# Kernel optimization log

Hardware: AMD Instinct MI355X
Metric: run time of the kernel (lower is better)

The kernel has to match this reference:

```python
import jax, jax.numpy as jnp
import numpy as np

B, N, D, Kp = 32, 4096, 128, 256  # batch*heads, seq_len, head_dim, linformer proj dim


def setup_inputs() -> dict:
    key = jax.random.key(0)
    ks = jax.random.split(key, 7)
    return {
        "Q": jax.random.normal(ks[0], (B, N, D), dtype=jnp.float32),
        "K": jax.random.normal(ks[1], (B, N, D), dtype=jnp.float32),
        "V": jax.random.normal(ks[2], (B, N, D), dtype=jnp.float32),
        "E_W": jax.random.normal(ks[3], (Kp, N), dtype=jnp.float32) * (1.0 / np.sqrt(N)),
        "E_b": jax.random.normal(ks[4], (Kp,), dtype=jnp.float32) * 0.02,
        "F_W": jax.random.normal(ks[5], (Kp, N), dtype=jnp.float32) * (1.0 / np.sqrt(N)),
        "F_b": jax.random.normal(ks[6], (Kp,), dtype=jnp.float32) * 0.02,
    }


def reference(Q, K, V, E_W, E_b, F_W, F_b):
    d = Q.shape[-1]
    scale = 1.0 / jnp.sqrt(jnp.asarray(d, Q.dtype))
    # E projection on K^T: [B,d,n] @ W^T -> [B,d,k]
    K_proj = jnp.einsum('bnd,kn->bdk', K, E_W) + E_b  # bias broadcasts over k axis
    # scaled scores [B,n,k], softmax over projected dim k
    scores = jnp.einsum('bnd,bdk->bnk', Q, K_proj) * scale
    P_bar = jax.nn.softmax(scores, axis=-1)
    # F projection on V^T then transpose back: [B,k,d]
    V_proj = jnp.einsum('bnd,kn->bkd', V, F_W) + F_b[:, None]
    # [B,n,k] @ [B,k,d] -> [B,n,d]
    return jnp.einsum('bnk,bkd->bnd', P_bar, V_proj)
```

## Files before the change

### kernel.cpp

```cpp
#include <hip/hip_runtime.h>
#include <cstdint>
#include <cstddef>

#define N_SEQ 4096
#define D_HEAD 128
#define KP_DIM 256

typedef __attribute__((ext_vector_type(4))) float f32x4;
typedef __attribute__((ext_vector_type(8))) short bf16x8;
typedef __attribute__((ext_vector_type(4))) short s16x4;
typedef __attribute__((ext_vector_type(2))) unsigned int u32x2;

static __device__ __forceinline__ short f2bf(float f) {
  uint32_t u = __builtin_bit_cast(uint32_t, f);
  u += 0x7FFFu + ((u >> 16) & 1u);
  return (short)(u >> 16);
}

static __device__ __forceinline__ unsigned int cvtpk(float a, float b) {
  unsigned int r;
  asm("v_cvt_pk_bf16_f32 %0, %1, %2" : "=v"(r) : "v"(a), "v"(b));
  return r;
}

static __device__ __forceinline__ int swz8(int r) { return (r ^ (r >> 2)) & 7; }

__global__ __launch_bounds__(256) void conv_w_kernel(
    const float* __restrict__ EW, const float* __restrict__ FW,
    short* __restrict__ wbf) {
  const int idx = blockIdx.x * 256 + threadIdx.x;
  const int half = 262144;
  f32x4 v = (idx < half) ? *(const f32x4*)(EW + (size_t)idx * 4)
                         : *(const f32x4*)(FW + (size_t)(idx - half) * 4);
  u32x2 h = {cvtpk(v[0], v[1]), cvtpk(v[2], v[3])};
  *(u32x2*)(wbf + (size_t)idx * 4) = h;
}

__global__ __launch_bounds__(1024, 4) void proj_partial_kernel(
    const float* __restrict__ Kin, const float* __restrict__ Vin,
    const short* __restrict__ wbf, float* __restrict__ pws) {
  const int bid = blockIdx.x;
  const int wk = (bid & 7) * 32 + (bid >> 3);
  const int b = wk & 31;
  const int s = (wk >> 5) & 3;
  const int p = wk >> 7;

  const float* __restrict__ X = (p == 0 ? Kin : Vin) + (size_t)b * (N_SEQ * D_HEAD);
  const short* __restrict__ wp = wbf + (size_t)p * (KP_DIM * N_SEQ);
  float* __restrict__ outp = pws + ((((size_t)b * 2 + p) * 4) + s) * (KP_DIM * D_HEAD);

  __shared__ __align__(16) short lw[2][KP_DIM * 64];
  __shared__ __align__(16) short xt[2][D_HEAD * 64];

  const int t = threadIdx.x;
  const int lane = t & 63;
  const int w = t >> 6;
  const int wkk = (w >> 1) * 32;
  const int wdd = (w & 1) * 64;
  const int l15 = lane & 15;
  const int l4 = lane >> 4;
  const int dq = t & 31;
  const int ng = t >> 5;

  const int n0 = s * 1024;

  f32x4 acc[2][4];
#pragma unroll
  for (int i = 0; i < 2; ++i)
#pragma unroll
    for (int j = 0; j < 4; ++j) acc[i][j] = (f32x4){0.f, 0.f, 0.f, 0.f};

  f32x4 xA[2], xB[2];

#define PROJ_WISSUE(BUF, NC)                                                        \
  do {                                                                              \
    _Pragma("unroll") for (int i_ = 0; i_ < 2; ++i_) {                              \
      int g_ = t + i_ * 1024;                                                       \
      int row_ = g_ >> 3, c_ = g_ & 7;                                              \
      __builtin_amdgcn_global_load_lds(                                             \
          (const __attribute__((address_space(1))) void*)(wp + (size_t)row_ * N_SEQ \
              + (NC) + ((c_ ^ swz8(row_)) << 3)),                                   \
          (__attribute__((address_space(3))) void*)(&lw[BUF][g_ * 8]), 16, 0, 0);   \
    }                                                                               \
  } while (0)

#define PROJ_XISSUE(XR, NC)                                                         \
  do {                                                                              \
    _Pragma("unroll") for (int i_ = 0; i_ < 2; ++i_)                                \
      XR[i_] = *(const f32x4*)(X + (size_t)((NC) + ng * 2 + i_) * D_HEAD + dq * 4); \
  } while (0)

#define PROJ_XCVT(XR, BUF)                                                          \
  do {                                                                              \
    _Pragma("unroll") for (int j_ = 0; j_ < 4; ++j_) {                              \
      int drow_ = dq * 4 + j_;                                                      \
      unsigned int hv_ = cvtpk(XR[0][j_], XR[1][j_]);                               \
      *(unsigned int*)(&xt[BUF][drow_ * 64 + ((ng * 2) ^ (swz8(drow_) << 3))]) = hv_; \
    }                                                                               \
  } while (0)

#define PROJ_COMPUTE(CUR)                                                           \
  do {                                                                              \
    _Pragma("unroll") for (int ks2 = 0; ks2 < 2; ++ks2) {                           \
      const int col0 = ks2 * 32 + l4 * 8;                                           \
      bf16x8 a_[2], bb_[4];                                                         \
      _Pragma("unroll") for (int mt = 0; mt < 2; ++mt) {                            \
        int row_ = wkk + mt * 16 + l15;                                             \
        a_[mt] = *(const bf16x8*)(&lw[CUR][row_ * 64 + (col0 ^ (swz8(row_) << 3))]); \
      }                                                                             \
      _Pragma("unroll") for (int nt = 0; nt < 4; ++nt) {                            \
        int row_ = wdd + nt * 16 + l15;                                             \
        bb_[nt] = *(const bf16x8*)(&xt[CUR][row_ * 64 + (col0 ^ (swz8(row_) << 3))]); \
      }                                                                             \
      _Pragma("unroll") for (int mt = 0; mt < 2; ++mt)                              \
        _Pragma("unroll") for (int nt = 0; nt < 4; ++nt)                            \
          acc[mt][nt] = __builtin_amdgcn_mfma_f32_16x16x32_bf16(a_[mt], bb_[nt],    \
                                                                acc[mt][nt], 0, 0, 0); \
    }                                                                               \
  } while (0)

  PROJ_XISSUE(xA, n0);
  PROJ_WISSUE(0, n0);
  asm volatile("s_waitcnt vmcnt(2)" ::: "memory");
  PROJ_XCVT(xA, 0);
  PROJ_XISSUE(xB, n0 + 64);
  asm volatile("s_waitcnt vmcnt(2)" ::: "memory");
  __syncthreads();

  for (int itp = 0; itp < 7; ++itp) {
    const int it0 = itp * 2;
    PROJ_WISSUE(1, n0 + (it0 + 1) * 64);
    PROJ_XISSUE(xA, n0 + (it0 + 2) * 64);
    PROJ_COMPUTE(0);
    asm volatile("s_waitcnt vmcnt(4)" ::: "memory");
    PROJ_XCVT(xB, 1);
    asm volatile("s_waitcnt vmcnt(2)" ::: "memory");
    __syncthreads();
    PROJ_WISSUE(0, n0 + (it0 + 2) * 64);
    PROJ_XISSUE(xB, n0 + (it0 + 3) * 64);
    PROJ_COMPUTE(1);
    asm volatile("s_waitcnt vmcnt(4)" ::: "memory");
    PROJ_XCVT(xA, 0);
    asm volatile("s_waitcnt vmcnt(2)" ::: "memory");
    __syncthreads();
  }
  PROJ_WISSUE(1, n0 + 15 * 64);
  PROJ_COMPUTE(0);
  asm volatile("s_waitcnt vmcnt(2)" ::: "memory");
  PROJ_XCVT(xB, 1);
  asm volatile("s_waitcnt vmcnt(0)" ::: "memory");
  __syncthreads();
  PROJ_COMPUTE(1);

#undef PROJ_WISSUE
#undef PROJ_XISSUE
#undef PROJ_XCVT
#undef PROJ_COMPUTE

#pragma unroll
  for (int mt = 0; mt < 2; ++mt)
#pragma unroll
    for (int nt = 0; nt < 4; ++nt)
#pragma unroll
      for (int r = 0; r < 4; ++r) {
        int kk = wkk + mt * 16 + l4 * 4 + r;
        int dd = wdd + nt * 16 + l15;
        outp[kk * D_HEAD + dd] = acc[mt][nt][r];
      }
}

__global__ __launch_bounds__(256) void reduce_bias_kernel(
    const float* __restrict__ pws, const float* __restrict__ Eb,
    const float* __restrict__ Fb, short* __restrict__ kp, short* __restrict__ vpt) {
  const int sub = blockIdx.x & 3;
  const int b = blockIdx.x >> 2;
  const int t = threadIdx.x;
  __shared__ short tile[128 * 128];
  if (sub < 2) {
    const float* __restrict__ base = pws + ((size_t)b * 2) * 4 * 32768;
    const int off = sub * 16384;
    for (int i = t; i < 16384; i += 256) {
      int ii = off + i;
      int k = ii >> 7;
      float v = base[ii] + base[ii + 32768] + base[ii + 65536] + base[ii + 98304] + Eb[k];
      kp[(size_t)b * 32768 + ii] = f2bf(v);
    }
  } else {
    const int kh = sub - 2;
    const float* __restrict__ base = pws + (((size_t)b * 2 + 1) * 4) * 32768 + kh * 16384;
    for (int i = t; i < 16384; i += 256) {
      int kl = i >> 7, d = i & 127;
      float v = base[i] + base[i + 32768] + base[i + 65536] + base[i + 98304] + Fb[kh * 128 + kl];
      tile[kl * 128 + (d ^ ((kl & 15) << 3))] = f2bf(v);
    }
    __syncthreads();
    for (int i = t; i < 16384; i += 256) {
      int d = i >> 7, kl = i & 127;
      vpt[(size_t)b * 32768 + d * 256 + kh * 128 + kl] = tile[kl * 128 + (d ^ ((kl & 15) << 3))];
    }
  }
}

__global__ __launch_bounds__(1024, 4) void attn_kernel(
    const float* __restrict__ Q, const short* __restrict__ kp,
    const short* __restrict__ vpt, float* __restrict__ out) {
  const int bid = blockIdx.x;
  const int wk = (bid & 7) * 32 + (bid >> 3);
  const int b = wk >> 3;
  const int slice = wk & 7;
  const int t = threadIdx.x;
  const int lane = t & 63;
  const int w = t >> 6;
  const int l15 = lane & 15, l4 = lane >> 4;

  __shared__ __align__(16) short lbuf[81920];
  short* lkp = lbuf;
  short* lvpt = lbuf + 32768;
  short* lpw = lbuf + 65536 + w * 1024;

  const short* __restrict__ kpb = kp + (size_t)b * 32768;
  const short* __restrict__ vptb = vpt + (size_t)b * 32768;

#pragma unroll
  for (int i = 0; i < 4; ++i) {
    int g = t + i * 1024;
    int row = g >> 4, c = g & 15;
    __builtin_amdgcn_global_load_lds(
        (const __attribute__((address_space(1))) void*)(kpb + (size_t)row * 128 +
                                                        ((c ^ (row & 7)) << 3)),
        (__attribute__((address_space(3))) void*)(&lkp[g * 8]), 16, 0, 0);
  }
#pragma unroll
  for (int i = 0; i < 4; ++i) {
    int g = t + i * 1024;
    int row = g >> 5, c = g & 31;
    __builtin_amdgcn_global_load_lds(
        (const __attribute__((address_space(1))) void*)(vptb + (size_t)row * 256 +
                                                        ((c ^ (row & 7)) << 3)),
        (__attribute__((address_space(3))) void*)(&lvpt[g * 8]), 16, 0, 0);
  }

  const float scale = 0.08838834764831845f;
  f32x4 qraw[8];
  {
    const float* qr = Q + ((size_t)b * N_SEQ + slice * 512 + w * 16 + l15) * D_HEAD;
#pragma unroll
    for (int ks = 0; ks < 4; ++ks) {
      qraw[2 * ks] = *(const f32x4*)(qr + ks * 32 + l4 * 8);
      qraw[2 * ks + 1] = *(const f32x4*)(qr + ks * 32 + l4 * 8 + 4);
    }
  }
  asm volatile("s_waitcnt vmcnt(0)" ::: "memory");
  __syncthreads();

#pragma unroll
  for (int rd = 0; rd < 2; ++rd) {
    const int rowBase = slice * 512 + rd * 256 + w * 16;

    bf16x8 qf[4];
#pragma unroll
    for (int ks = 0; ks < 4; ++ks) {
      union { unsigned int u[4]; bf16x8 v; } cv;
      cv.u[0] = cvtpk(qraw[2 * ks][0] * scale, qraw[2 * ks][1] * scale);
      cv.u[1] = cvtpk(qraw[2 * ks][2] * scale, qraw[2 * ks][3] * scale);
      cv.u[2] = cvtpk(qraw[2 * ks + 1][0] * scale, qraw[2 * ks + 1][1] * scale);
      cv.u[3] = cvtpk(qraw[2 * ks + 1][2] * scale, qraw[2 * ks + 1][3] * scale);
      qf[ks] = cv.v;
    }

    f32x4 accs[16];
#pragma unroll
    for (int i = 0; i < 16; ++i) accs[i] = (f32x4){0.f, 0.f, 0.f, 0.f};
#pragma unroll
    for (int ks = 0; ks < 4; ++ks) {
#pragma unroll
      for (int nt = 0; nt < 16; ++nt) {
        bf16x8 af = *(const bf16x8*)(&lkp[(nt * 16 + l15) * 128 +
                                          (((ks * 4 + l4) ^ (l15 & 7)) << 3)]);
        accs[nt] = __builtin_amdgcn_mfma_f32_16x16x32_bf16(af, qf[ks], accs[nt], 0, 0, 0);
      }
    }

    float m = -1e30f;
#pragma unroll
    for (int nt = 0; nt < 16; ++nt)
#pragma unroll
      for (int r = 0; r < 4; ++r) m = fmaxf(m, accs[nt][r]);
    m = fmaxf(m, __shfl_xor(m, 16));
    m = fmaxf(m, __shfl_xor(m, 32));
    float s = 0.f;
#pragma unroll
    for (int nt = 0; nt < 16; ++nt)
#pragma unroll
      for (int r = 0; r < 4; ++r) {
        float e = __expf(accs[nt][r] - m);
        accs[nt][r] = e;
        s += e;
      }
    s += __shfl_xor(s, 16);
    s += __shfl_xor(s, 32);
    float inv = 1.0f / s;

    f32x4 acco[8];
#pragma unroll
    for (int i = 0; i < 8; ++i) acco[i] = (f32x4){0.f, 0.f, 0.f, 0.f};
#pragma unroll
    for (int qq = 0; qq < 4; ++qq) {
#pragma unroll
      for (int ntl = 0; ntl < 4; ++ntl) {
        int nt = qq * 4 + ntl;
        int cw = 2 * ntl + (l4 >> 1);
        unsigned int p0 = cvtpk(accs[nt][0] * inv, accs[nt][1] * inv);
        unsigned int p1 = cvtpk(accs[nt][2] * inv, accs[nt][3] * inv);
        *(u32x2*)((char*)lpw + l15 * 128 + ((cw ^ (l15 & 7)) << 4) + (l4 & 1) * 8) =
            (u32x2){p0, p1};
      }
      if (rd == 0 && qq == 3) {
        const float* qr = Q + ((size_t)b * N_SEQ + slice * 512 + 256 + w * 16 + l15) * D_HEAD;
#pragma unroll
        for (int ks = 0; ks < 4; ++ks) {
          qraw[2 * ks] = *(const f32x4*)(qr + ks * 32 + l4 * 8);
          qraw[2 * ks + 1] = *(const f32x4*)(qr + ks * 32 + l4 * 8 + 4);
        }
      }
#pragma unroll
      for (int ksl = 0; ksl < 2; ++ksl) {
        bf16x8 pa = *(const bf16x8*)((char*)lpw + l15 * 128 +
                                     (((4 * ksl + l4) ^ (l15 & 7)) << 4));
        int ksa = qq * 2 + ksl;
#pragma unroll
        for (int ntv = 0; ntv < 8; ++ntv) {
          bf16x8 av = *(const bf16x8*)(&lvpt[(ntv * 16 + l15) * 256 +
                                             (((ksa * 4 + l4) ^ (l15 & 7)) << 3)]);
          acco[ntv] = __builtin_amdgcn_mfma_f32_16x16x32_bf16(av, pa, acco[ntv], 0, 0, 0);
        }
      }
    }

    float* ob = out + ((size_t)b * N_SEQ + rowBase) * D_HEAD;
#pragma unroll
    for (int ntv = 0; ntv < 8; ++ntv)
      *(f32x4*)(ob + (size_t)l15 * D_HEAD + ntv * 16 + l4 * 4) = acco[ntv];
  }
}

extern "C" void kernel_launch(void* const* d_in, const int* in_sizes, int n_in,
                              void* d_out, int out_size, void* d_ws, size_t ws_size,
                              hipStream_t stream) {
  const float* Q  = (const float*)d_in[0];
  const float* K  = (const float*)d_in[1];
  const float* V  = (const float*)d_in[2];
  const float* EW = (const float*)d_in[3];
  const float* Eb = (const float*)d_in[4];
  const float* FW = (const float*)d_in[5];
  const float* Fb = (const float*)d_in[6];
  float* out = (float*)d_out;

  short* wbf = (short*)d_out;
  float* pws = (float*)d_out + 2097152;
  short* kpb = (short*)d_ws;
  short* vpt = (short*)((char*)d_ws + (size_t)32 * KP_DIM * D_HEAD * 2);

  conv_w_kernel<<<dim3(2048), dim3(256), 0, stream>>>(EW, FW, wbf);
  proj_partial_kernel<<<dim3(256), dim3(1024), 0, stream>>>(K, V, wbf, pws);
  reduce_bias_kernel<<<dim3(128), dim3(256), 0, stream>>>(pws, Eb, Fb, kpb, vpt);
  attn_kernel<<<dim3(256), dim3(1024), 0, stream>>>(Q, kpb, vpt, out);
}
```

Measured before the change: 95.13 us.

## Load projection weights directly to registers and split K-dim across wave halves

The projection kernel no longer stages the bf16 weight tile in LDS. Each wave now loads its weight fragments straight from global memory into registers. Waves are split into two halves that each cover half of every 64-wide sequence chunk over a 64x64 output tile, and the two partial sums are merged through LDS at the end. This frees a large amount of shared memory and removes LDS traffic for the weights. In exchange, the weight loads are no longer swizzled or shared across waves, there are more accumulator registers per wave, and the merge step adds extra synchronisation.

```diff
diff --git a/kernel.cpp b/kernel.cpp
--- a/kernel.cpp
+++ b/kernel.cpp
@@ -8,7 +8,6 @@
 
 typedef __attribute__((ext_vector_type(4))) float f32x4;
 typedef __attribute__((ext_vector_type(8))) short bf16x8;
-typedef __attribute__((ext_vector_type(4))) short s16x4;
 typedef __attribute__((ext_vector_type(2))) unsigned int u32x2;
 
 static __device__ __forceinline__ short f2bf(float f) {
@@ -49,14 +48,17 @@
   const short* __restrict__ wp = wbf + (size_t)p * (KP_DIM * N_SEQ);
   float* __restrict__ outp = pws + ((((size_t)b * 2 + p) * 4) + s) * (KP_DIM * D_HEAD);
 
-  __shared__ __align__(16) short lw[2][KP_DIM * 64];
   __shared__ __align__(16) short xt[2][D_HEAD * 64];
+  __shared__ __align__(16) float mrg[2][64 * 64];
 
   const int t = threadIdx.x;
   const int lane = t & 63;
   const int w = t >> 6;
-  const int wkk = (w >> 1) * 32;
-  const int wdd = (w & 1) * 64;
+  const int slot = w & 7;
+  const int half = w >> 3;
+  const int wkk = (slot >> 1) * 64;
+  const int wdd = (slot & 1) * 64;
+  const int nh = half * 32;
   const int l15 = lane & 15;
   const int l4 = lane >> 4;
   const int dq = t & 31;
@@ -64,25 +66,13 @@
 
   const int n0 = s * 1024;
 
-  f32x4 acc[2][4];
-#pragma unroll
-  for (int i = 0; i < 2; ++i)
+  f32x4 acc[4][4];
+#pragma unroll
+  for (int i = 0; i < 4; ++i)
 #pragma unroll
     for (int j = 0; j < 4; ++j) acc[i][j] = (f32x4){0.f, 0.f, 0.f, 0.f};
 
   f32x4 xA[2], xB[2];
-
-#define PROJ_WISSUE(BUF, NC)                                                        \
-  do {                                                                              \
-    _Pragma("unroll") for (int i_ = 0; i_ < 2; ++i_) {                              \
-      int g_ = t + i_ * 1024;                                                       \
-      int row_ = g_ >> 3, c_ = g_ & 7;                                              \
-      __builtin_amdgcn_global_load_lds(                                             \
-          (const __attribute__((address_space(1))) void*)(wp + (size_t)row_ * N_SEQ \
-              + (NC) + ((c_ ^ swz8(row_)) << 3)),                                   \
-          (__attribute__((address_space(3))) void*)(&lw[BUF][g_ * 8]), 16, 0, 0);   \
-    }                                                                               \
-  } while (0)
 
 #define PROJ_XISSUE(XR, NC)                                                         \
   do {                                                                              \
@@ -99,74 +89,117 @@
     }                                                                               \
   } while (0)
 
-#define PROJ_COMPUTE(CUR)                                                           \
+#define PROJ_WLOAD(WA, NN)                                                          \
   do {                                                                              \
-    _Pragma("unroll") for (int ks2 = 0; ks2 < 2; ++ks2) {                           \
-      const int col0 = ks2 * 32 + l4 * 8;                                           \
-      bf16x8 a_[2], bb_[4];                                                         \
-      _Pragma("unroll") for (int mt = 0; mt < 2; ++mt) {                            \
-        int row_ = wkk + mt * 16 + l15;                                             \
-        a_[mt] = *(const bf16x8*)(&lw[CUR][row_ * 64 + (col0 ^ (swz8(row_) << 3))]); \
-      }                                                                             \
-      _Pragma("unroll") for (int nt = 0; nt < 4; ++nt) {                            \
-        int row_ = wdd + nt * 16 + l15;                                             \
-        bb_[nt] = *(const bf16x8*)(&xt[CUR][row_ * 64 + (col0 ^ (swz8(row_) << 3))]); \
-      }                                                                             \
-      _Pragma("unroll") for (int mt = 0; mt < 2; ++mt)                              \
-        _Pragma("unroll") for (int nt = 0; nt < 4; ++nt)                            \
-          acc[mt][nt] = __builtin_amdgcn_mfma_f32_16x16x32_bf16(a_[mt], bb_[nt],    \
-                                                                acc[mt][nt], 0, 0, 0); \
+    _Pragma("unroll") for (int mt_ = 0; mt_ < 4; ++mt_)                             \
+      WA[mt_] = *(const bf16x8*)(wp + (size_t)(wkk + mt_ * 16 + l15) * N_SEQ +      \
+                                 (NN) + nh + l4 * 8);                               \
+  } while (0)
+
+#define PROJ_COMPUTE(CUR, WA)                                                       \
+  do {                                                                              \
+    bf16x8 bb_[4];                                                                  \
+    _Pragma("unroll") for (int nt_ = 0; nt_ < 4; ++nt_) {                           \
+      int row_ = wdd + nt_ * 16 + l15;                                              \
+      bb_[nt_] = *(const bf16x8*)(&xt[CUR][row_ * 64 +                              \
+                                           ((nh + l4 * 8) ^ (swz8(row_) << 3))]);   \
     }                                                                               \
+    _Pragma("unroll") for (int mt_ = 0; mt_ < 4; ++mt_)                             \
+      _Pragma("unroll") for (int nt_ = 0; nt_ < 4; ++nt_)                           \
+        acc[mt_][nt_] = __builtin_amdgcn_mfma_f32_16x16x32_bf16(WA[mt_], bb_[nt_],  \
+                                                                acc[mt_][nt_], 0, 0, 0); \
   } while (0)
 
   PROJ_XISSUE(xA, n0);
-  PROJ_WISSUE(0, n0);
-  asm volatile("s_waitcnt vmcnt(2)" ::: "memory");
+  asm volatile("s_waitcnt vmcnt(0)" ::: "memory");
   PROJ_XCVT(xA, 0);
   PROJ_XISSUE(xB, n0 + 64);
-  asm volatile("s_waitcnt vmcnt(2)" ::: "memory");
   __syncthreads();
 
   for (int itp = 0; itp < 7; ++itp) {
     const int it0 = itp * 2;
-    PROJ_WISSUE(1, n0 + (it0 + 1) * 64);
-    PROJ_XISSUE(xA, n0 + (it0 + 2) * 64);
-    PROJ_COMPUTE(0);
-    asm volatile("s_waitcnt vmcnt(4)" ::: "memory");
+    {
+      const int nn = n0 + it0 * 64;
+      bf16x8 wa[4];
+      PROJ_WLOAD(wa, nn);
+      PROJ_XISSUE(xA, nn + 128);
+      asm volatile("s_waitcnt vmcnt(2)" ::: "memory");
+      PROJ_XCVT(xB, 1);
+      PROJ_COMPUTE(0, wa);
+      __syncthreads();
+    }
+    {
+      const int nn = n0 + (it0 + 1) * 64;
+      bf16x8 wa[4];
+      PROJ_WLOAD(wa, nn);
+      PROJ_XISSUE(xB, nn + 128);
+      asm volatile("s_waitcnt vmcnt(2)" ::: "memory");
+      PROJ_XCVT(xA, 0);
+      PROJ_COMPUTE(1, wa);
+      __syncthreads();
+    }
+  }
+  {
+    const int nn = n0 + 14 * 64;
+    bf16x8 wa[4];
+    PROJ_WLOAD(wa, nn);
+    asm volatile("s_waitcnt vmcnt(0)" ::: "memory");
     PROJ_XCVT(xB, 1);
-    asm volatile("s_waitcnt vmcnt(2)" ::: "memory");
+    PROJ_COMPUTE(0, wa);
     __syncthreads();
-    PROJ_WISSUE(0, n0 + (it0 + 2) * 64);
-    PROJ_XISSUE(xB, n0 + (it0 + 3) * 64);
-    PROJ_COMPUTE(1);
-    asm volatile("s_waitcnt vmcnt(4)" ::: "memory");
-    PROJ_XCVT(xA, 0);
-    asm volatile("s_waitcnt vmcnt(2)" ::: "memory");
-    __syncthreads();
-  }
-  PROJ_WISSUE(1, n0 + 15 * 64);
-  PROJ_COMPUTE(0);
-  asm volatile("s_waitcnt vmcnt(2)" ::: "memory");
-  PROJ_XCVT(xB, 1);
-  asm volatile("s_waitcnt vmcnt(0)" ::: "memory");
-  __syncthreads();
-  PROJ_COMPUTE(1);
-
-#undef PROJ_WISSUE
+  }
+  {
+    const int nn = n0 + 15 * 64;
+    bf16x8 wa[4];
+    PROJ_WLOAD(wa, nn);
+    asm volatile("s_waitcnt vmcnt(0)" ::: "memory");
+    PROJ_COMPUTE(1, wa);
+  }
+
 #undef PROJ_XISSUE
 #undef PROJ_XCVT
+#undef PROJ_WLOAD
 #undef PROJ_COMPUTE
 
-#pragma unroll
-  for (int mt = 0; mt < 2; ++mt)
-#pragma unroll
-    for (int nt = 0; nt < 4; ++nt)
-#pragma unroll
-      for (int r = 0; r < 4; ++r) {
-        int kk = wkk + mt * 16 + l4 * 4 + r;
-        int dd = wdd + nt * 16 + l15;
-        outp[kk * D_HEAD + dd] = acc[mt][nt][r];
-      }
+  __syncthreads();
+#pragma unroll
+  for (int ph = 0; ph < 4; ++ph) {
+    if (half == 1 && (slot >> 1) == ph) {
+      float* m = &mrg[slot & 1][0];
+#pragma unroll
+      for (int mt = 0; mt < 4; ++mt)
+#pragma unroll
+        for (int nt = 0; nt < 4; ++nt)
+#pragma unroll
+          for (int r = 0; r < 4; ++r)
+            m[(mt * 16 + l4 * 4 + r) * 64 + nt * 16 + l15] = acc[mt][nt][r];
+    }
+    __syncthreads();
+    if (half == 0 && (slot >> 1) == ph) {
+      const float* m = &mrg[slot & 1][0];
+#pragma unroll
+      for (int mt = 0; mt < 4; ++mt)
+#pragma unroll
+        for (int nt = 0; nt < 4; ++nt)
+#pragma unroll
+          for (int r = 0; r < 4; ++r)
+            acc[mt][nt][r] += m[(mt * 16 + l4 * 4 + r) * 64 + nt * 16 + l15];
+    }
+    __syncthreads();
+  }
+
+  if (half == 0) {
+#pragma unroll
+    for (int mt = 0; mt < 4; ++mt)
+#pragma unroll
+      for (int nt = 0; nt < 4; ++nt)
+#pragma unroll
+        for (int r = 0; r < 4; ++r) {
+          int kk = wkk + mt * 16 + l4 * 4 + r;
+          int dd = wdd + nt * 16 + l15;
+          outp[kk * D_HEAD + dd] = acc[mt][nt][r];
+        }
+  }
 }
 
 __global__ __launch_bounds__(256) void reduce_bias_kernel(
```

Result: slower. 120.1 us (+26.3%).
